# Kernel optimization log

Hardware: AMD Instinct MI355X
Metric: run time of the kernel (lower is better)

Reference implementation:

```python
import jax, jax.numpy as jnp
import numpy as np

BSZ, N, E, D = 8, 1024, 49152, 256
K, ALPHA = 10, 0.1
EDGE_RATIO, NODE_RATIO = 0.8, 0.7
K_NODES = int(np.ceil(NODE_RATIO * N))  # torch_geometric topk uses ceil -> 717


def setup_inputs() -> dict:
    key = jax.random.key(0)
    ks = jax.random.split(key, 10)
    concept_hidden = jax.random.normal(ks[0], (BSZ, N, D), jnp.float32)
    head = jax.random.randint(ks[1], (BSZ, E), 0, N, jnp.int32)
    off = jax.random.randint(ks[2], (BSZ, E), 1, N, jnp.int32)
    tail = ((head + off) % N).astype(jnp.int32)  # guaranteed no self-loops
    triple_label = jnp.ones((BSZ, E), jnp.int32)  # all edges valid (no -1 padding)
    relation_hidden = jnp.zeros((BSZ, 1), jnp.float32)  # unused by the math
    concept_labels = jax.random.randint(ks[3], (BSZ, N), 0, 3, jnp.int32)
    concept_ids = jax.random.randint(ks[4], (BSZ, N), 0, 50000, jnp.int32)
    # PageRank temp (learnable param, deterministic init from alpha/K)
    t = ALPHA * (1.0 - ALPHA) ** np.arange(K + 1)
    t[-1] = (1.0 - ALPHA) ** K
    temp = jnp.asarray(t, jnp.float32)
    # GraphAttention params (heads=1)
    g = float(np.sqrt(6.0 / (D + D)))
    W_proj = jax.random.uniform(ks[5], (D, D), jnp.float32, -g, g)
    ga = float(np.sqrt(6.0 / (1 + D)))
    a_src = jax.random.uniform(ks[6], (D,), jnp.float32, -ga, ga)
    a_tgt = jax.random.uniform(ks[7], (D,), jnp.float32, -ga, ga)
    # output Linear(2D -> D)
    gl = float(np.sqrt(1.0 / (2 * D)))
    W_lin = jax.random.uniform(ks[8], (D, 2 * D), jnp.float32, -gl, gl)
    b_lin = jax.random.uniform(ks[9], (D,), jnp.float32, -gl, gl)
    return dict(concept_hidden=concept_hidden, relation_hidden=relation_hidden,
                head=head, tail=tail, triple_label=triple_label,
                concept_labels=concept_labels, concept_ids=concept_ids,
                temp=temp, W_proj=W_proj, a_src=a_src, a_tgt=a_tgt,
                W_lin=W_lin, b_lin=b_lin)


def _per_sample(x, h, t, labels, ids, temp, W_proj, a_src, a_tgt, W_lin, b_lin):
    # ---- PageRank (gcn_norm with added self-loops, aggr='add' into tail) ----
    sl = jnp.arange(N, dtype=jnp.int32)
    hs = jnp.concatenate([h, sl])
    ts = jnp.concatenate([t, sl])
    deg = jax.ops.segment_sum(jnp.ones(E + N, x.dtype), ts, num_segments=N)
    dinv = jnp.where(deg > 0, jax.lax.rsqrt(deg), 0.0)
    norm = dinv[hs] * dinv[ts]  # [E+N]

    def step(xk, gamma):
        xk = jax.ops.segment_sum(norm[:, None] * xk[hs], ts, num_segments=N)
        return xk, gamma * xk

    _, contribs = jax.lax.scan(step, x, temp[1:])  # K steps
    x_cut = temp[0] * x + contribs.sum(0)  # [N, D]

    # ---- edge attention (GAT-style scoring, sigmoid) ----
    proj = x_cut @ W_proj.T                       # [N, D] (heads=1)
    s_src = proj @ a_src                          # [N]
    s_tgt = proj @ a_tgt                          # [N]
    attn = jax.nn.sigmoid(s_src[h] + s_tgt[t])    # [E]

    # ---- symmetrize + coalesce(mean), done densely ----
    rows = jnp.concatenate([h, t])
    cols = jnp.concatenate([t, h])
    vals = jnp.concatenate([attn, attn])
    S = jnp.zeros((N, N), x.dtype).at[rows, cols].add(vals)
    Cn = jnp.zeros((N, N), x.dtype).at[rows, cols].add(1.0)
    valid = Cn > 0
    A = jnp.where(valid, S / jnp.maximum(Cn, 1.0), 0.0)  # coalesced mean adjacency

    # ---- np.percentile(attn, 20) with linear interpolation over valid edges ----
    sv = jnp.sort(jnp.where(valid, A, jnp.inf).reshape(-1))  # valid values first
    M = valid.sum()
    pos = (1.0 - EDGE_RATIO) * (M.astype(x.dtype) - 1.0)
    lo = jnp.floor(pos).astype(jnp.int32)
    frac = pos - lo.astype(x.dtype)
    hi = jnp.minimum(lo + 1, M - 1)  # stays within the finite (valid) prefix
    cut = sv[lo] + frac * (sv[hi] - sv[lo])

    A_cut = jnp.where(valid & (A >= cut), A, 0.0)  # edges below percentile zeroed

    # ---- node scoring: scatter_add of attn*x[src] into dst == A_cut^T @ x ----
    out = A_cut.T @ x                              # [N, D]
    score = jnp.abs(out).sum(1) + 1e-7             # [N]
    _, perm = jax.lax.top_k(score, K_NODES)

    pooled = A_cut[perm] @ x                       # [k, D]
    hcat = jnp.concatenate([x[perm], pooled], axis=-1)  # [k, 2D]
    h_new = hcat @ W_lin.T + b_lin                 # [k, D]
    return h_new, labels[perm], ids[perm]


def reference(concept_hidden, relation_hidden, head, tail, triple_label,
              concept_labels, concept_ids, temp, W_proj, a_src, a_tgt,
              W_lin, b_lin):
    f = jax.vmap(_per_sample,
                 in_axes=(0, 0, 0, 0, 0, None, None, None, None, None, None))
    return f(concept_hidden, head, tail, concept_labels, concept_ids,
             temp, W_proj, a_src, a_tgt, W_lin, b_lin)
```

## Files before the change

### kernel.cpp

```cpp
#include <hip/hip_runtime.h>
#include <math.h>

#define BSZ 8
#define NN 1024
#define EE 49152
#define DD 256
#define KSTEPS 10
#define NCH 192
#define KNODES 717
#define RS 256
#define MROWS 720
#define CSTRIDE 131072
#define SELB 64

typedef __attribute__((ext_vector_type(8))) short short8_t;
typedef __attribute__((ext_vector_type(4))) float f32x4;

__device__ __forceinline__ void fma4(float4& a, float w, const float4 v) {
    a.x += w * v.x; a.y += w * v.y; a.z += w * v.z; a.w += w * v.w;
}

__device__ __forceinline__ unsigned short f2bf(float f) {
    unsigned u = __float_as_uint(f);
    u = (u + 0x7fffu + ((u >> 16) & 1u)) >> 16;
    return (unsigned short)u;
}


__global__ void k_hist(const int* __restrict__ head, const int* __restrict__ tail,
                       int* __restrict__ cnt_t, int* __restrict__ cnt_h,
                       const float* __restrict__ Wl, unsigned short* __restrict__ Wb) {
    __shared__ int lt[NN];
    __shared__ int lh[NN];
    int tid = threadIdx.x;
    if (blockIdx.x >= BSZ * NCH) {
        int i = (blockIdx.x - BSZ * NCH) * 256 + tid;
        Wb[i] = f2bf(Wl[i]);
        return;
    }
    int b = blockIdx.x / NCH, ch = blockIdx.x % NCH;
    for (int i = tid; i < NN; i += 256) { lt[i] = 0; lh[i] = 0; }
    __syncthreads();
    int e = ch * 256 + tid;
    int h = head[b * EE + e], t = tail[b * EE + e];
    atomicAdd(&lt[t], 1);
    atomicAdd(&lh[h], 1);
    __syncthreads();
    int base = (b * NCH + ch) * NN;
    for (int i = tid; i < NN; i += 256) { cnt_t[base + i] = lt[i]; cnt_h[base + i] = lh[i]; }
}

__global__ void k_chunkscan(int* __restrict__ cnt_t, int* __restrict__ cnt_h,
                            int* __restrict__ tot_t, int* __restrict__ tot_h,
                            float* __restrict__ dinv) {
    int gid = blockIdx.x * 256 + threadIdx.x;
    int which = gid >> 13;
    int i = gid & 8191;
    int b = i >> 10, n = i & 1023;
    int* c = which ? cnt_h : cnt_t;
    int run = 0;
    for (int s = 0; s < NCH; s++) {
        int idx = (b * NCH + s) * NN + n;
        int v = c[idx];
        c[idx] = run;
        run += v;
    }
    (which ? tot_h : tot_t)[i] = run;
    if (!which) dinv[i] = 1.0f / sqrtf((float)(run + 1));
}

__global__ __launch_bounds__(1024) void k_nodescan(const int* __restrict__ tot_t,
                                                   const int* __restrict__ tot_h,
                                                   int* __restrict__ toff, int* __restrict__ hoff) {
    __shared__ int sb[NN];
    int b = blockIdx.x >> 1, which = blockIdx.x & 1;
    int tid = threadIdx.x;
    const int* tot = which ? tot_h : tot_t;
    int* off = which ? hoff : toff;
    int v = tot[b * NN + tid];
    sb[tid] = v;
    __syncthreads();
    for (int o = 1; o < NN; o <<= 1) {
        int t = (tid >= o) ? sb[tid - o] : 0;
        __syncthreads();
        sb[tid] += t;
        __syncthreads();
    }
    off[b * (NN + 1) + tid] = sb[tid] - v;
    if (tid == NN - 1) off[b * (NN + 1) + NN] = sb[tid];
}

__global__ void k_fill(const int* __restrict__ head, const int* __restrict__ tail,
                       const int* __restrict__ cnt_t, const int* __restrict__ cnt_h,
                       const int* __restrict__ toff, const int* __restrict__ hoff,
                       const float* __restrict__ dinv,
                       int* __restrict__ t_head, float* __restrict__ t_norm, int* __restrict__ t_eidx,
                       int* __restrict__ h_tail, int* __restrict__ h_eidx) {
    __shared__ int sh[256], st[256];
    int b = blockIdx.x / NCH, ch = blockIdx.x % NCH;
    int tid = threadIdx.x;
    int e = ch * 256 + tid;
    int h = head[b * EE + e], t = tail[b * EE + e];
    sh[tid] = h;
    st[tid] = t;
    __syncthreads();
    int rt = 0, rh = 0;
    for (int j = 0; j < tid; j++) {
        rt += (st[j] == t);
        rh += (sh[j] == h);
    }
    int post = toff[b * (NN + 1) + t] + cnt_t[(b * NCH + ch) * NN + t] + rt;
    t_head[b * EE + post] = h;
    t_norm[b * EE + post] = dinv[b * NN + h] * dinv[b * NN + t];
    t_eidx[b * EE + post] = e;
    int posh = hoff[b * (NN + 1) + h] + cnt_h[(b * NCH + ch) * NN + h] + rh;
    h_tail[b * EE + posh] = t;
    h_eidx[b * EE + posh] = e;
}

__global__ __launch_bounds__(256) void k_prstep(const float* __restrict__ src, float* __restrict__ dst,
                         float* __restrict__ xacc, const float* __restrict__ temp,
                         const int* __restrict__ toff, const int* __restrict__ t_head,
                         const float* __restrict__ t_norm, const float* __restrict__ dinv,
                         int kidx,
                         const float* __restrict__ Wp, const float* __restrict__ as_,
                         const float* __restrict__ at_, float* __restrict__ vsrc,
                         float* __restrict__ vtgt) {
    if (blockIdx.x >= BSZ * NN / 4) {
        int d = threadIdx.x;
        float vs = 0.f, vt = 0.f;
        for (int i = 0; i < DD; i++) {
            float w = Wp[i * DD + d];
            vs += as_[i] * w;
            vt += at_[i] * w;
        }
        vsrc[d] = vs;
        vtgt[d] = vt;
        return;
    }
    int wid = threadIdx.x >> 6, lane = threadIdx.x & 63;
    int b = blockIdx.x & 7;
    int n = (blockIdx.x >> 3) * 4 + wid;
    int g = b * NN + n;
    int o0 = __builtin_amdgcn_readfirstlane(toff[b * (NN + 1) + n]);
    int o1 = __builtin_amdgcn_readfirstlane(toff[b * (NN + 1) + n + 1]);
    int ebase = __builtin_amdgcn_readfirstlane(b * EE);
    const int* __restrict__ hp = t_head + ebase;
    const float* __restrict__ wp = t_norm + ebase;
    float dv = dinv[g];
    const float4* src4 = (const float4*)src;
    size_t r4 = (size_t)g * 64 + lane;
    size_t bb = (size_t)b * NN * 64;
    float4 sv = src4[r4];
    float sl = dv * dv;
    float4 acc;
    acc.x = sl * sv.x; acc.y = sl * sv.y; acc.z = sl * sv.z; acc.w = sl * sv.w;
    int j = o0;
    for (; j + 8 <= o1; j += 8) {
        int c0 = hp[j], c1 = hp[j + 1], c2 = hp[j + 2], c3 = hp[j + 3];
        int c4 = hp[j + 4], c5 = hp[j + 5], c6 = hp[j + 6], c7 = hp[j + 7];
        float w0 = wp[j], w1 = wp[j + 1], w2 = wp[j + 2], w3 = wp[j + 3];
        float w4 = wp[j + 4], w5 = wp[j + 5], w6 = wp[j + 6], w7 = wp[j + 7];
        float4 xa = src4[bb + (size_t)c0 * 64 + lane];
        float4 xb = src4[bb + (size_t)c1 * 64 + lane];
        float4 xc = src4[bb + (size_t)c2 * 64 + lane];
        float4 xd = src4[bb + (size_t)c3 * 64 + lane];
        float4 xe = src4[bb + (size_t)c4 * 64 + lane];
        float4 xf = src4[bb + (size_t)c5 * 64 + lane];
        float4 xg = src4[bb + (size_t)c6 * 64 + lane];
        float4 xh = src4[bb + (size_t)c7 * 64 + lane];
        fma4(acc, w0, xa); fma4(acc, w1, xb); fma4(acc, w2, xc); fma4(acc, w3, xd);
        fma4(acc, w4, xe); fma4(acc, w5, xf); fma4(acc, w6, xg); fma4(acc, w7, xh);
    }
    for (; j + 4 <= o1; j += 4) {
        int c0 = hp[j], c1 = hp[j + 1], c2 = hp[j + 2], c3 = hp[j + 3];
        float w0 = wp[j], w1 = wp[j + 1], w2 = wp[j + 2], w3 = wp[j + 3];
        float4 xa = src4[bb + (size_t)c0 * 64 + lane];
        float4 xb = src4[bb + (size_t)c1 * 64 + lane];
        float4 xc = src4[bb + (size_t)c2 * 64 + lane];
        float4 xd = src4[bb + (size_t)c3 * 64 + lane];
        fma4(acc, w0, xa); fma4(acc, w1, xb); fma4(acc, w2, xc); fma4(acc, w3, xd);
    }
    for (; j < o1; j++) {
        int c0 = hp[j];
        float w0 = wp[j];
        float4 xa = src4[bb + (size_t)c0 * 64 + lane];
        fma4(acc, w0, xa);
    }
    ((float4*)dst)[r4] = acc;
    float gm = temp[kidx + 1];
    float4 xa2;
    if (kidx == 0) {
        float t0 = temp[0];
        xa2.x = t0 * sv.x; xa2.y = t0 * sv.y; xa2.z = t0 * sv.z; xa2.w = t0 * sv.w;
    } else {
        xa2 = ((float4*)xacc)[r4];
    }
    fma4(xa2, gm, acc);
    ((float4*)xacc)[r4] = xa2;
}


__global__ void k_s(const float* __restrict__ xacc, const float* __restrict__ vsrc,
                    const float* __restrict__ vtgt, float* __restrict__ ssrc,
                    float* __restrict__ stgt) {
    int g = blockIdx.x * 4 + (threadIdx.x >> 6);
    int lane = threadIdx.x & 63;
    const float4* xr = (const float4*)(xacc + (size_t)g * DD);
    float4 xv = xr[lane];
    float4 vs = ((const float4*)vsrc)[lane];
    float4 vt = ((const float4*)vtgt)[lane];
    float s1 = xv.x * vs.x + xv.y * vs.y + xv.z * vs.z + xv.w * vs.w;
    float s2 = xv.x * vt.x + xv.y * vt.y + xv.z * vt.z + xv.w * vt.w;
    for (int o = 32; o > 0; o >>= 1) {
        s1 += __shfl_down(s1, o);
        s2 += __shfl_down(s2, o);
    }
    if (lane == 0) {
        ssrc[g] = s1;
        stgt[g] = s2;
    }
}

__global__ void k_attn(const int* __restrict__ head, const int* __restrict__ tail,
                       const float* __restrict__ ssrc, const float* __restrict__ stgt,
                       float* __restrict__ attn) {
    int i = blockIdx.x * 256 + threadIdx.x;
    int b = i / EE;
    int h = head[i], t = tail[i];
    float z = ssrc[b * NN + h] + stgt[b * NN + t];
    attn[i] = 1.0f / (1.0f + expf(-z));
}


__global__ __launch_bounds__(256) void k_rowbuild(const int* __restrict__ hoff, const int* __restrict__ h_tail,
                          const int* __restrict__ h_eidx, const int* __restrict__ toff,
                          const int* __restrict__ t_head, const int* __restrict__ t_eidx,
                          const float* __restrict__ attn,
                          int* __restrict__ rcol, float* __restrict__ rval,
                          int* __restrict__ nnzrow,
                          float* __restrict__ cvals, int* __restrict__ ccount) {
    __shared__ int cols[RS];
    __shared__ float vals[RS];
    __shared__ int first[NN];
    __shared__ int cntb[NN];
    __shared__ int rankv[NN];
    __shared__ int ssum[256];
    __shared__ int cbase;
    int g = blockIdx.x;
    int b = g >> 10, n = g & 1023;
    int tid = threadIdx.x;
    int a0 = hoff[b * (NN + 1) + n], a1 = hoff[b * (NN + 1) + n + 1];
    int c0 = toff[b * (NN + 1) + n], c1 = toff[b * (NN + 1) + n + 1];
    int kh = a1 - a0;
    int kk = kh + (c1 - c0);
    if (kk > RS) kk = RS;
    for (int i = tid; i < NN; i += 256) { first[i] = 0x7fffffff; cntb[i] = 0; }
    __syncthreads();
    if (tid < kk) {
        int c, e;
        if (tid < kh) { c = h_tail[b * EE + a0 + tid]; e = h_eidx[b * EE + a0 + tid]; }
        else          { c = t_head[b * EE + c0 + (tid - kh)]; e = t_eidx[b * EE + c0 + (tid - kh)]; }
        cols[tid] = c;
        vals[tid] = attn[b * EE + e];
        atomicMin(&first[c], tid);
        atomicAdd(&cntb[c], 1);
    }
    __syncthreads();
    int i0 = tid * 4;
    int p0 = (first[i0] != 0x7fffffff);
    int p1 = (first[i0 + 1] != 0x7fffffff);
    int p2 = (first[i0 + 2] != 0x7fffffff);
    int p3 = (first[i0 + 3] != 0x7fffffff);
    int psum = p0 + p1 + p2 + p3;
    ssum[tid] = psum;
    __syncthreads();
    for (int o = 1; o < 256; o <<= 1) {
        int t = (tid >= o) ? ssum[tid - o] : 0;
        __syncthreads();
        ssum[tid] += t;
        __syncthreads();
    }
    int run = ssum[tid] - psum;
    rankv[i0] = run;            run += p0;
    rankv[i0 + 1] = run;        run += p1;
    rankv[i0 + 2] = run;        run += p2;
    rankv[i0 + 3] = run;
    int total = ssum[255];
    if (tid == 0) cbase = atomicAdd(&ccount[b], total);
    __syncthreads();
    if (tid < kk) {
        int c = cols[tid];
        if (first[c] == tid) {
            int cc = cntb[c];
            float v;
            if (cc == 1) {
                v = vals[tid];
            } else {
                float s = 0.f;
                for (int j = tid; j < kk; j++)
                    if (cols[j] == c) s += vals[j];
                v = s / (float)cc;
            }
            int r = rankv[c];
            size_t rb = ((size_t)g << 8) + r;
            rcol[rb] = c;
            rval[rb] = v;
            cvals[(size_t)b * CSTRIDE + cbase + r] = v;
        }
    }
    if (tid == 0) nnzrow[g] = total;
}


__global__ void k_selinit(const int* __restrict__ ccount, int* __restrict__ sel) {
    int b = threadIdx.x;
    if (b < BSZ) {
        int M = ccount[b];
        float pos = 0.2f * ((float)M - 1.0f);
        int lo = (int)floorf(pos);
        float frac = pos - (float)lo;
        sel[b * 8 + 0] = lo;
        sel[b * 8 + 1] = min(lo + 1, M - 1);
        sel[b * 8 + 2] = 0;
        sel[b * 8 + 3] = 0;
        sel[b * 8 + 4] = __float_as_int(frac);
    }
}

__global__ void k_selhist(const float* __restrict__ cv, const int* __restrict__ ccount,
                          const int* __restrict__ sel, int* __restrict__ hist, int pass) {
    __shared__ int lh[512];
    int tid = threadIdx.x;
    lh[tid] = 0;
    lh[tid + 256] = 0;
    __syncthreads();
    int b = blockIdx.x / SELB, blk = blockIdx.x % SELB;
    int M = ccount[b];
    const float* vp = cv + (size_t)b * CSTRIDE;
    unsigned p0 = (unsigned)sel[b * 8 + 2];
    unsigned p1 = (unsigned)sel[b * 8 + 3];
    int shift = 24 - 8 * pass;
    for (int i = blk * 256 + tid; i < M; i += SELB * 256) {
        unsigned bits = __float_as_uint(vp[i]);
        unsigned bucket = (bits >> shift) & 255u;
        if (pass == 0) {
            atomicAdd(&lh[bucket], 1);
            atomicAdd(&lh[256 + bucket], 1);
        } else {
            unsigned hb = bits >> (shift + 8);
            if (hb == p0) atomicAdd(&lh[bucket], 1);
            if (hb == p1) atomicAdd(&lh[256 + bucket], 1);
        }
    }
    __syncthreads();
    int v0 = lh[tid];
    if (v0) atomicAdd(&hist[(b * 2 + 0) * 256 + tid], v0);
    int v1 = lh[tid + 256];
    if (v1) atomicAdd(&hist[(b * 2 + 1) * 256 + tid], v1);
}

__global__ void k_selreduce(int* __restrict__ hist, int* __restrict__ sel) {
    __shared__ int sb[256];
    int b = blockIdx.x >> 1, ch = blockIdx.x & 1;
    int tid = threadIdx.x;
    int idx = (b * 2 + ch) * 256 + tid;
    int v = hist[idx];
    hist[idx] = 0;
    int rem = sel[b * 8 + ch];
    int pref = sel[b * 8 + 2 + ch];
    sb[tid] = v;
    __syncthreads();
    for (int o = 1; o < 256; o <<= 1) {
        int t = (tid >= o) ? sb[tid - o] : 0;
        __syncthreads();
        sb[tid] += t;
        __syncthreads();
    }
    int excl = sb[tid] - v;
    if (v > 0 && rem >= excl && rem < excl + v) {
        sel[b * 8 + ch] = rem - excl;
        sel[b * 8 + 2 + ch] = (pref << 8) | tid;
    }
}

__global__ void k_cut(const int* __restrict__ sel, float* __restrict__ cut) {
    int b = threadIdx.x;
    if (b < BSZ) {
        float v0 = __uint_as_float((unsigned)sel[b * 8 + 2]);
        float v1 = __uint_as_float((unsigned)sel[b * 8 + 3]);
        float frac = __int_as_float(sel[b * 8 + 4]);
        cut[b] = v0 + frac * (v1 - v0);
    }
}


__global__ __launch_bounds__(256) void k_outscore(const int* __restrict__ rcol, const float* __restrict__ rval,
                           const int* __restrict__ nnzrow, const float* __restrict__ x,
                           const float* __restrict__ cut, float* __restrict__ out_pr,
                           float* __restrict__ score) {
    int wid = threadIdx.x >> 6, lane = threadIdx.x & 63;
    int b = blockIdx.x & 7;
    int n = (blockIdx.x >> 3) * 4 + wid;
    int g = b * NN + n;
    float cb = cut[b];
    int nnz = __builtin_amdgcn_readfirstlane(nnzrow[g]);
    int rbase = __builtin_amdgcn_readfirstlane(g << 8);
    const int* __restrict__ cp = rcol + rbase;
    const float* __restrict__ vp = rval + rbase;
    const float4* x4 = (const float4*)x;
    size_t bb = (size_t)b * NN * 64;
    float4 acc = make_float4(0.f, 0.f, 0.f, 0.f);
    int j = 0;
    for (; j + 4 <= nnz; j += 4) {
        float a0 = vp[j], a1 = vp[j + 1], a2 = vp[j + 2], a3 = vp[j + 3];
        int c0 = cp[j], c1 = cp[j + 1], c2 = cp[j + 2], c3 = cp[j + 3];
        float4 xa = x4[bb + (size_t)c0 * 64 + lane];
        float4 xb = x4[bb + (size_t)c1 * 64 + lane];
        float4 xc = x4[bb + (size_t)c2 * 64 + lane];
        float4 xd = x4[bb + (size_t)c3 * 64 + lane];
        if (a0 >= cb) fma4(acc, a0, xa);
        if (a1 >= cb) fma4(acc, a1, xb);
        if (a2 >= cb) fma4(acc, a2, xc);
        if (a3 >= cb) fma4(acc, a3, xd);
    }
    for (; j < nnz; j++) {
        float a0 = vp[j];
        int c0 = cp[j];
        float4 xa = x4[bb + (size_t)c0 * 64 + lane];
        if (a0 >= cb) fma4(acc, a0, xa);
    }
    ((float4*)out_pr)[(size_t)g * 64 + lane] = acc;
    float4 r;
    r.x = fabsf(acc.x); r.y = fabsf(acc.y); r.z = fabsf(acc.z); r.w = fabsf(acc.w);
    for (int o = 32; o > 0; o >>= 1) {
        r.x += __shfl_down(r.x, o);
        r.y += __shfl_down(r.y, o);
        r.z += __shfl_down(r.z, o);
        r.w += __shfl_down(r.w, o);
    }
    r.x += r.z;
    r.y += r.w;
    r.x += r.y;
    if (lane == 0) score[g] = r.x + 1e-7f;
}


__global__ __launch_bounds__(1024) void k_topk(const float* __restrict__ score,
                                               const int* __restrict__ labels,
                                               const int* __restrict__ ids,
                                               int* __restrict__ perm,
                                               float* __restrict__ out_lab,
                                               float* __restrict__ out_ids) {
    __shared__ float sc[NN];
    __shared__ int idx[NN];
    int b = blockIdx.x, tid = threadIdx.x;
    sc[tid] = score[b * NN + tid];
    idx[tid] = tid;
    __syncthreads();
    for (int k = 2; k <= NN; k <<= 1) {
        for (int j = k >> 1; j > 0; j >>= 1) {
            int p = tid ^ j;
            if (p > tid) {
                float s0 = sc[tid], s1 = sc[p];
                int i0 = idx[tid], i1 = idx[p];
                bool before01 = (s0 > s1) || (s0 == s1 && i0 < i1);
                bool up = ((tid & k) == 0);
                bool sw = up ? (!before01) : before01;
                if (sw) {
                    sc[tid] = s1; sc[p] = s0;
                    idx[tid] = i1; idx[p] = i0;
                }
            }
            __syncthreads();
        }
    }
    perm[b * NN + tid] = idx[tid];
    if (tid < KNODES) {
        int p = idx[tid];
        out_lab[b * KNODES + tid] = (float)labels[b * NN + p];
        out_ids[b * KNODES + tid] = (float)ids[b * NN + p];
    }
}


__global__ void k_packA(const float* __restrict__ x, const float* __restrict__ outpr,
                        const int* __restrict__ perm, unsigned short* __restrict__ A16) {
    int row = blockIdx.x;
    int b = row / MROWS, i = row - b * MROWS;
    int tid = threadIdx.x;
    size_t ob = (size_t)row * 512;
    if (i < KNODES) {
        int p = perm[b * NN + i];
        float v0 = x[((size_t)(b * NN + p)) * DD + tid];
        float v1 = outpr[((size_t)(b * NN + p)) * DD + tid];
        A16[ob + tid] = f2bf(v0);
        A16[ob + 256 + tid] = f2bf(v1);
    } else {
        A16[ob + tid] = 0;
        A16[ob + 256 + tid] = 0;
    }
}

__global__ __launch_bounds__(256) void k_hnew_mfma(const unsigned short* __restrict__ A16,
                                                   const unsigned short* __restrict__ Wb,
                                                   const float* __restrict__ b_lin,
                                                   float* __restrict__ hnew) {
    int w = blockIdx.x * 4 + (threadIdx.x >> 6);
    int lane = threadIdx.x & 63;
    int b = w / (45 * 16);
    int rem = w - b * (45 * 16);
    int mt = rem >> 4, nt = rem & 15;
    int m = lane & 15, quad = lane >> 4;
    const unsigned short* ap = A16 + ((size_t)(b * MROWS + mt * 16 + m) * 512 + quad * 8);
    const unsigned short* bp = Wb + ((size_t)(nt * 16 + m) * 512 + quad * 8);
    f32x4 acc = {0.f, 0.f, 0.f, 0.f};
#pragma unroll
    for (int s = 0; s < 16; s++) {
        short8_t av = *(const short8_t*)(ap + s * 32);
        short8_t bv = *(const short8_t*)(bp + s * 32);
        acc = __builtin_amdgcn_mfma_f32_16x16x32_bf16(av, bv, acc, 0, 0, 0);
    }
    int d = nt * 16 + m;
    float bl = b_lin[d];
#pragma unroll
    for (int r = 0; r < 4; r++) {
        int i = mt * 16 + quad * 4 + r;
        if (i < KNODES) hnew[((size_t)(b * KNODES + i)) * DD + d] = acc[r] + bl;
    }
}


extern "C" void kernel_launch(void* const* d_in, const int* in_sizes, int n_in,
                              void* d_out, int out_size, void* d_ws, size_t ws_size,
                              hipStream_t stream) {
    const float* x      = (const float*)d_in[0];
    const int*   head   = (const int*)d_in[2];
    const int*   tail   = (const int*)d_in[3];
    const int*   labels = (const int*)d_in[5];
    const int*   ids    = (const int*)d_in[6];
    const float* temp   = (const float*)d_in[7];
    const float* Wp     = (const float*)d_in[8];
    const float* asrc   = (const float*)d_in[9];
    const float* atgt   = (const float*)d_in[10];
    const float* Wl     = (const float*)d_in[11];
    const float* blin   = (const float*)d_in[12];

    float* out_h   = (float*)d_out;
    float* out_lab = out_h + (size_t)BSZ * KNODES * DD;
    float* out_ids = out_lab + (size_t)BSZ * KNODES;

    size_t o = 0;
    char* ws = (char*)d_ws;
    auto A_ = [&](size_t bytes) -> void* {
        void* p = ws + o;
        o += (bytes + 255) & ~(size_t)255;
        return p;
    };
    int*   cnt_t  = (int*)  A_((size_t)BSZ * NCH * NN * 4);
    int*   cnt_h  = (int*)  A_((size_t)BSZ * NCH * NN * 4);
    int*   tot_t  = (int*)  A_((size_t)BSZ * NN * 4);
    int*   tot_h  = (int*)  A_((size_t)BSZ * NN * 4);
    int*   toff   = (int*)  A_((size_t)BSZ * (NN + 1) * 4);
    int*   hoff   = (int*)  A_((size_t)BSZ * (NN + 1) * 4);
    float* dinv   = (float*)A_((size_t)BSZ * NN * 4);
    int*   t_head = (int*)  A_((size_t)BSZ * EE * 4);
    float* t_norm = (float*)A_((size_t)BSZ * EE * 4);
    int*   t_eidx = (int*)  A_((size_t)BSZ * EE * 4);
    int*   h_tail = (int*)  A_((size_t)BSZ * EE * 4);
    int*   h_eidx = (int*)  A_((size_t)BSZ * EE * 4);
    float* xkA    = (float*)A_((size_t)BSZ * NN * DD * 4);
    float* xkB    = (float*)A_((size_t)BSZ * NN * DD * 4);
    float* xacc   = (float*)A_((size_t)BSZ * NN * DD * 4);
    float* vsrc   = (float*)A_(DD * 4);
    float* vtgt   = (float*)A_(DD * 4);
    float* ssrc   = (float*)A_((size_t)BSZ * NN * 4);
    float* stgt   = (float*)A_((size_t)BSZ * NN * 4);
    float* attn   = (float*)A_((size_t)BSZ * EE * 4);
    int*   rcol   = (int*)  A_((size_t)BSZ * NN * RS * 4);
    float* rval   = (float*)A_((size_t)BSZ * NN * RS * 4);
    int*   nnzrow = (int*)  A_((size_t)BSZ * NN * 4);
    float* cvals  = (float*)A_((size_t)BSZ * CSTRIDE * 4);
    int*   ccount = (int*)  A_(BSZ * 4);
    int*   sel    = (int*)  A_(BSZ * 8 * 4);
    int*   hist   = (int*)  A_(BSZ * 2 * 256 * 4);
    float* cutv   = (float*)A_(BSZ * 4);
    float* outpr  = (float*)A_((size_t)BSZ * NN * DD * 4);
    float* scorev = (float*)A_((size_t)BSZ * NN * 4);
    int*   perm   = (int*)  A_((size_t)BSZ * NN * 4);
    unsigned short* Wb16 = (unsigned short*)A_((size_t)DD * 512 * 2);
    unsigned short* A16  = (unsigned short*)A_((size_t)BSZ * MROWS * 512 * 2);
    if (o > ws_size) return;

    hipMemsetAsync(ccount, 0, BSZ * 4, stream);
    hipMemsetAsync(hist, 0, BSZ * 2 * 256 * 4, stream);

    k_hist<<<BSZ * NCH + 512, 256, 0, stream>>>(head, tail, cnt_t, cnt_h, Wl, Wb16);
    k_chunkscan<<<64, 256, 0, stream>>>(cnt_t, cnt_h, tot_t, tot_h, dinv);
    k_nodescan<<<16, 1024, 0, stream>>>(tot_t, tot_h, toff, hoff);
    k_fill<<<BSZ * NCH, 256, 0, stream>>>(head, tail, cnt_t, cnt_h, toff, hoff, dinv,
                                          t_head, t_norm, t_eidx, h_tail, h_eidx);
    for (int k = 0; k < KSTEPS; k++) {
        const float* src = (k == 0) ? x : ((k & 1) ? xkA : xkB);
        float* dst = (k & 1) ? xkB : xkA;
        int grid = BSZ * NN / 4 + ((k == KSTEPS - 1) ? 1 : 0);
        k_prstep<<<grid, 256, 0, stream>>>(src, dst, xacc, temp, toff, t_head, t_norm, dinv, k,
                                           Wp, asrc, atgt, vsrc, vtgt);
    }
    k_s<<<BSZ * NN / 4, 256, 0, stream>>>(xacc, vsrc, vtgt, ssrc, stgt);
    k_attn<<<BSZ * EE / 256, 256, 0, stream>>>(head, tail, ssrc, stgt, attn);
    k_rowbuild<<<BSZ * NN, 256, 0, stream>>>(hoff, h_tail, h_eidx, toff, t_head, t_eidx,
                                             attn, rcol, rval, nnzrow, cvals, ccount);
    k_selinit<<<1, 64, 0, stream>>>(ccount, sel);
    for (int p = 0; p < 4; p++) {
        k_selhist<<<BSZ * SELB, 256, 0, stream>>>(cvals, ccount, sel, hist, p);
        k_selreduce<<<16, 256, 0, stream>>>(hist, sel);
    }
    k_cut<<<1, 64, 0, stream>>>(sel, cutv);
    k_outscore<<<BSZ * NN / 4, 256, 0, stream>>>(rcol, rval, nnzrow, x, cutv, outpr, scorev);
    k_topk<<<BSZ, 1024, 0, stream>>>(scorev, labels, ids, perm, out_lab, out_ids);
    k_packA<<<BSZ * MROWS, 256, 0, stream>>>(x, outpr, perm, A16);
    k_hnew_mfma<<<BSZ * 45 * 16 / 4, 256, 0, stream>>>(A16, Wb16, blin, out_h);
}
```

Baseline: 521.2 us.

## Fuse attention sigmoid into rowbuild and replace rank scan with bitmask popcount

The separate k_attn kernel is removed. Edge attention is now computed inside k_rowbuild directly from the node scores ssrc/stgt, so the eidx permutation arrays and the attn buffer are no longer written or read. The 1024-entry shared-memory prefix scan used to rank distinct columns is replaced by a 32-word presence bitmask with popcounts, which removes many barriers. The tradeoff is that each edge's sigmoid may be computed more than once, and each thread runs a short serial popcount loop to find its rank.

```diff
diff --git a/kernel.cpp b/kernel.cpp
--- a/kernel.cpp
+++ b/kernel.cpp
@@ -94,8 +94,8 @@
                        const int* __restrict__ cnt_t, const int* __restrict__ cnt_h,
                        const int* __restrict__ toff, const int* __restrict__ hoff,
                        const float* __restrict__ dinv,
-                       int* __restrict__ t_head, float* __restrict__ t_norm, int* __restrict__ t_eidx,
-                       int* __restrict__ h_tail, int* __restrict__ h_eidx) {
+                       int* __restrict__ t_head, float* __restrict__ t_norm,
+                       int* __restrict__ h_tail) {
     __shared__ int sh[256], st[256];
     int b = blockIdx.x / NCH, ch = blockIdx.x % NCH;
     int tid = threadIdx.x;
@@ -112,10 +112,8 @@
     int post = toff[b * (NN + 1) + t] + cnt_t[(b * NCH + ch) * NN + t] + rt;
     t_head[b * EE + post] = h;
     t_norm[b * EE + post] = dinv[b * NN + h] * dinv[b * NN + t];
-    t_eidx[b * EE + post] = e;
     int posh = hoff[b * (NN + 1) + h] + cnt_h[(b * NCH + ch) * NN + h] + rh;
     h_tail[b * EE + posh] = t;
-    h_eidx[b * EE + posh] = e;
 }
 
 __global__ __launch_bounds__(256) void k_prstep(const float* __restrict__ src, float* __restrict__ dst,
@@ -222,21 +220,10 @@
     }
 }
 
-__global__ void k_attn(const int* __restrict__ head, const int* __restrict__ tail,
-                       const float* __restrict__ ssrc, const float* __restrict__ stgt,
-                       float* __restrict__ attn) {
-    int i = blockIdx.x * 256 + threadIdx.x;
-    int b = i / EE;
-    int h = head[i], t = tail[i];
-    float z = ssrc[b * NN + h] + stgt[b * NN + t];
-    attn[i] = 1.0f / (1.0f + expf(-z));
-}
-
 
 __global__ __launch_bounds__(256) void k_rowbuild(const int* __restrict__ hoff, const int* __restrict__ h_tail,
-                          const int* __restrict__ h_eidx, const int* __restrict__ toff,
-                          const int* __restrict__ t_head, const int* __restrict__ t_eidx,
-                          const float* __restrict__ attn,
+                          const int* __restrict__ toff, const int* __restrict__ t_head,
+                          const float* __restrict__ ssrc, const float* __restrict__ stgt,
                           int* __restrict__ rcol, float* __restrict__ rval,
                           int* __restrict__ nnzrow,
                           float* __restrict__ cvals, int* __restrict__ ccount) {
@@ -244,8 +231,7 @@
     __shared__ float vals[RS];
     __shared__ int first[NN];
     __shared__ int cntb[NN];
-    __shared__ int rankv[NN];
-    __shared__ int ssum[256];
+    __shared__ unsigned pres[32];
     __shared__ int cbase;
     int g = blockIdx.x;
     int b = g >> 10, n = g & 1023;
@@ -255,39 +241,29 @@
     int kh = a1 - a0;
     int kk = kh + (c1 - c0);
     if (kk > RS) kk = RS;
-    for (int i = tid; i < NN; i += 256) { first[i] = 0x7fffffff; cntb[i] = 0; }
+    ((int4*)first)[tid] = make_int4(0x7fffffff, 0x7fffffff, 0x7fffffff, 0x7fffffff);
+    ((int4*)cntb)[tid] = make_int4(0, 0, 0, 0);
+    if (tid < 32) pres[tid] = 0;
+    float sn = ssrc[g], tn = stgt[g];
     __syncthreads();
     if (tid < kk) {
-        int c, e;
-        if (tid < kh) { c = h_tail[b * EE + a0 + tid]; e = h_eidx[b * EE + a0 + tid]; }
-        else          { c = t_head[b * EE + c0 + (tid - kh)]; e = t_eidx[b * EE + c0 + (tid - kh)]; }
+        int c;
+        float z;
+        if (tid < kh) { c = h_tail[b * EE + a0 + tid]; z = sn + stgt[b * NN + c]; }
+        else          { c = t_head[b * EE + c0 + (tid - kh)]; z = ssrc[b * NN + c] + tn; }
         cols[tid] = c;
-        vals[tid] = attn[b * EE + e];
+        vals[tid] = 1.0f / (1.0f + expf(-z));
         atomicMin(&first[c], tid);
         atomicAdd(&cntb[c], 1);
-    }
-    __syncthreads();
-    int i0 = tid * 4;
-    int p0 = (first[i0] != 0x7fffffff);
-    int p1 = (first[i0 + 1] != 0x7fffffff);
-    int p2 = (first[i0 + 2] != 0x7fffffff);
-    int p3 = (first[i0 + 3] != 0x7fffffff);
-    int psum = p0 + p1 + p2 + p3;
-    ssum[tid] = psum;
-    __syncthreads();
-    for (int o = 1; o < 256; o <<= 1) {
-        int t = (tid >= o) ? ssum[tid - o] : 0;
-        __syncthreads();
-        ssum[tid] += t;
-        __syncthreads();
-    }
-    int run = ssum[tid] - psum;
-    rankv[i0] = run;            run += p0;
-    rankv[i0 + 1] = run;        run += p1;
-    rankv[i0 + 2] = run;        run += p2;
-    rankv[i0 + 3] = run;
-    int total = ssum[255];
-    if (tid == 0) cbase = atomicAdd(&ccount[b], total);
+        atomicOr(&pres[c >> 5], 1u << (c & 31));
+    }
+    __syncthreads();
+    if (tid == 0) {
+        int tot = 0;
+        for (int w = 0; w < 32; w++) tot += __popc(pres[w]);
+        nnzrow[g] = tot;
+        cbase = atomicAdd(&ccount[b], tot);
+    }
     __syncthreads();
     if (tid < kk) {
         int c = cols[tid];
@@ -302,14 +278,15 @@
                     if (cols[j] == c) s += vals[j];
                 v = s / (float)cc;
             }
-            int r = rankv[c];
+            int w = c >> 5;
+            int r = __popc(pres[w] & ((1u << (c & 31)) - 1u));
+            for (int u = 0; u < w; u++) r += __popc(pres[u]);
             size_t rb = ((size_t)g << 8) + r;
             rcol[rb] = c;
             rval[rb] = v;
             cvals[(size_t)b * CSTRIDE + cbase + r] = v;
         }
     }
-    if (tid == 0) nnzrow[g] = total;
 }
 
 
@@ -566,9 +543,7 @@
     float* dinv   = (float*)A_((size_t)BSZ * NN * 4);
     int*   t_head = (int*)  A_((size_t)BSZ * EE * 4);
     float* t_norm = (float*)A_((size_t)BSZ * EE * 4);
-    int*   t_eidx = (int*)  A_((size_t)BSZ * EE * 4);
     int*   h_tail = (int*)  A_((size_t)BSZ * EE * 4);
-    int*   h_eidx = (int*)  A_((size_t)BSZ * EE * 4);
     float* xkA    = (float*)A_((size_t)BSZ * NN * DD * 4);
     float* xkB    = (float*)A_((size_t)BSZ * NN * DD * 4);
     float* xacc   = (float*)A_((size_t)BSZ * NN * DD * 4);
@@ -576,7 +551,6 @@
     float* vtgt   = (float*)A_(DD * 4);
     float* ssrc   = (float*)A_((size_t)BSZ * NN * 4);
     float* stgt   = (float*)A_((size_t)BSZ * NN * 4);
-    float* attn   = (float*)A_((size_t)BSZ * EE * 4);
     int*   rcol   = (int*)  A_((size_t)BSZ * NN * RS * 4);
     float* rval   = (float*)A_((size_t)BSZ * NN * RS * 4);
     int*   nnzrow = (int*)  A_((size_t)BSZ * NN * 4);
@@ -599,7 +573,7 @@
     k_chunkscan<<<64, 256, 0, stream>>>(cnt_t, cnt_h, tot_t, tot_h, dinv);
     k_nodescan<<<16, 1024, 0, stream>>>(tot_t, tot_h, toff, hoff);
     k_fill<<<BSZ * NCH, 256, 0, stream>>>(head, tail, cnt_t, cnt_h, toff, hoff, dinv,
-                                          t_head, t_norm, t_eidx, h_tail, h_eidx);
+                                          t_head, t_norm, h_tail);
     for (int k = 0; k < KSTEPS; k++) {
         const float* src = (k == 0) ? x : ((k & 1) ? xkA : xkB);
         float* dst = (k & 1) ? xkB : xkA;
@@ -608,9 +582,8 @@
                                            Wp, asrc, atgt, vsrc, vtgt);
     }
     k_s<<<BSZ * NN / 4, 256, 0, stream>>>(xacc, vsrc, vtgt, ssrc, stgt);
-    k_attn<<<BSZ * EE / 256, 256, 0, stream>>>(head, tail, ssrc, stgt, attn);
-    k_rowbuild<<<BSZ * NN, 256, 0, stream>>>(hoff, h_tail, h_eidx, toff, t_head, t_eidx,
-                                             attn, rcol, rval, nnzrow, cvals, ccount);
+    k_rowbuild<<<BSZ * NN, 256, 0, stream>>>(hoff, h_tail, toff, t_head, ssrc, stgt,
+                                             rcol, rval, nnzrow, cvals, ccount);
     k_selinit<<<1, 64, 0, stream>>>(ccount, sel);
     for (int p = 0; p < 4; p++) {
         k_selhist<<<BSZ * SELB, 256, 0, stream>>>(cvals, ccount, sel, hist, p);
```

Result: faster. 508.1 us (-2.5%).
